# Kernel optimization log

Hardware: AMD Instinct MI355X
Metric: run time of the kernel (lower is better)

Reference implementation:

```python
import jax, jax.numpy as jnp
import numpy as np

EPS = jnp.finfo(jnp.float32).eps


def setup_inputs() -> dict:
    key = jax.random.key(0)
    k0, k1, k2 = jax.random.split(key, 3)
    B, N = 1, 4194304
    cloud_t0 = jax.random.normal(k0, (B, N, 3), dtype=jnp.float32)
    cloud_t1 = jax.random.normal(k1, (B, N, 3), dtype=jnp.float32)
    weights = jax.random.uniform(k2, (B, N), dtype=jnp.float32)
    return {"cloud_t0": cloud_t0, "cloud_t1": cloud_t1, "weights": weights}


def reference(cloud_t0, cloud_t1, weights):
    # use_epsilon_on_weights = False branch
    count_nonzero = jnp.sum(weights > 0.0, axis=-1)
    not_enough_points = count_nonzero < 3
    weights = weights + (not_enough_points.astype(weights.dtype) * EPS)[:, None]

    cum_wts = jnp.sum(weights, axis=-1)                      # (B,)
    w = weights[:, :, None]                                   # (B,N,1)
    mx = jnp.sum(cloud_t0 * w, axis=1) / cum_wts[:, None]     # (B,3) weighted centroid
    my = jnp.sum(cloud_t1 * w, axis=1) / cum_wts[:, None]
    Xc = cloud_t0 - mx[:, None, :]
    Yc = cloud_t1 - my[:, None, :]
    # weighted cross-covariance: (B,3,3)
    Sxy = jnp.einsum('bno,bni->boi', Yc * w, Xc) / cum_wts[:, None, None]

    U, D, Vh = jnp.linalg.svd(Sxy, full_matrices=False)       # torch.svd returns V = Vh^T
    V = jnp.swapaxes(Vh, -1, -2)

    # rank via torch.linalg.matrix_rank default tol: max_sv * max(m,n) * eps
    tol = D.max(axis=-1) * 3 * EPS
    rank = jnp.sum(D > tol[:, None], axis=-1)

    det_S = jnp.linalg.det(Sxy)
    det_mul = jnp.linalg.det(U) * jnp.linalg.det(V)
    sign_full = jnp.where(det_S < 0.0, -1.0, 1.0)             # rank == 3 case
    sign_def = jnp.where(jnp.isclose(det_mul, -1.0), -1.0, 1.0)  # rank == 2 case
    s = jnp.where(rank > 2, sign_full, sign_def)              # (B,)

    # R = U @ diag(1,1,s) @ V^T
    diag = jnp.stack([jnp.ones_like(s), jnp.ones_like(s), s], axis=-1)  # (B,3)
    R = jnp.einsum('boc,bc,bic->boi', U, diag, V)             # (B,3,3)
    t = my - jnp.einsum('boc,bc->bo', R, mx)                  # (B,3)

    B = R.shape[0]
    R4 = jnp.concatenate([R, jnp.zeros((B, 1, 3), R.dtype)], axis=1)    # (B,4,3)
    t4 = jnp.concatenate([t, jnp.ones((B, 1), t.dtype)], axis=-1)       # (B,4)
    T = jnp.concatenate([R4, t4[:, :, None]], axis=-1)        # (B,4,4)
    return T, not_enough_points
```

## Files before the change

### kernel.cpp

```cpp
#include <hip/hip_runtime.h>
#include <math.h>

#define NACC 32
#define NMAIN 17
#define NFALL 15

__device__ __forceinline__ void accum_main(float w, float x0, float x1, float x2,
                                           float y0, float y1, float y2, float* a) {
    a[0] += (w > 0.0f) ? 1.0f : 0.0f;
    a[1] += w;
    a[2] = fmaf(w, x0, a[2]); a[3] = fmaf(w, x1, a[3]); a[4] = fmaf(w, x2, a[4]);
    float wy0 = w * y0, wy1 = w * y1, wy2 = w * y2;
    a[5] += wy0; a[6] += wy1; a[7] += wy2;
    a[8]  = fmaf(wy0, x0, a[8]);  a[9]  = fmaf(wy0, x1, a[9]);  a[10] = fmaf(wy0, x2, a[10]);
    a[11] = fmaf(wy1, x0, a[11]); a[12] = fmaf(wy1, x1, a[12]); a[13] = fmaf(wy1, x2, a[13]);
    a[14] = fmaf(wy2, x0, a[14]); a[15] = fmaf(wy2, x1, a[15]); a[16] = fmaf(wy2, x2, a[16]);
}

__device__ __forceinline__ void accum_fall(float x0, float x1, float x2,
                                           float y0, float y1, float y2, float* f) {
    f[0] += x0; f[1] += x1; f[2] += x2;
    f[3] += y0; f[4] += y1; f[5] += y2;
    f[6]  = fmaf(y0, x0, f[6]);  f[7]  = fmaf(y0, x1, f[7]);  f[8]  = fmaf(y0, x2, f[8]);
    f[9]  = fmaf(y1, x0, f[9]);  f[10] = fmaf(y1, x1, f[10]); f[11] = fmaf(y1, x2, f[11]);
    f[12] = fmaf(y2, x0, f[12]); f[13] = fmaf(y2, x1, f[13]); f[14] = fmaf(y2, x2, f[14]);
}

__device__ __forceinline__ void accum_group_main(float4 wv, float4 x0, float4 x1, float4 x2,
                                                 float4 y0, float4 y1, float4 y2, float* a) {
    accum_main(wv.x, x0.x, x0.y, x0.z, y0.x, y0.y, y0.z, a);
    accum_main(wv.y, x0.w, x1.x, x1.y, y0.w, y1.x, y1.y, a);
    accum_main(wv.z, x1.z, x1.w, x2.x, y1.z, y1.w, y2.x, a);
    accum_main(wv.w, x2.y, x2.z, x2.w, y2.y, y2.z, y2.w, a);
}

__device__ __forceinline__ void accum_group_fall(float4 x0, float4 x1, float4 x2,
                                                 float4 y0, float4 y1, float4 y2, float* f) {
    accum_fall(x0.x, x0.y, x0.z, y0.x, y0.y, y0.z, f);
    accum_fall(x0.w, x1.x, x1.y, y0.w, y1.x, y1.y, f);
    accum_fall(x1.z, x1.w, x2.x, y1.z, y1.w, y2.x, f);
    accum_fall(x2.y, x2.z, x2.w, y2.y, y2.z, y2.w, f);
}

template <int NV>
__device__ __forceinline__ void block_reduce(float* v, float (*sm)[NACC], int t) {
    int wave = t >> 6, lane = t & 63;
    #pragma unroll
    for (int off = 32; off > 0; off >>= 1) {
        #pragma unroll
        for (int i = 0; i < NV; ++i) v[i] += __shfl_down(v[i], off, 64);
    }
    if (lane == 0) {
        #pragma unroll
        for (int i = 0; i < NV; ++i) sm[wave][i] = v[i];
    }
    __syncthreads();
}

__global__ __launch_bounds__(256) void kabsch_reduce(
    const float* __restrict__ c0, const float* __restrict__ c1,
    const float* __restrict__ w, int N, float* __restrict__ partials, int nblocks) {
    __shared__ float sm[4][NACC];

    float a[NMAIN];
    #pragma unroll
    for (int i = 0; i < NMAIN; ++i) a[i] = 0.0f;

    const int t = threadIdx.x;
    const int tid = blockIdx.x * blockDim.x + t;
    const int nthreads = gridDim.x * blockDim.x;
    const int ngroups = N >> 2;
    const float4* A4 = (const float4*)c0;
    const float4* B4 = (const float4*)c1;
    const float4* W4 = (const float4*)w;

    int g = tid;
    bool have = g < ngroups;
    float4 cw, ca0, ca1, ca2, cb0, cb1, cb2;
    if (have) {
        size_t b = (size_t)3 * (size_t)g;
        cw = W4[g];
        ca0 = A4[b]; ca1 = A4[b + 1]; ca2 = A4[b + 2];
        cb0 = B4[b]; cb1 = B4[b + 1]; cb2 = B4[b + 2];
    }
    while (have) {
        int gn = g + nthreads;
        bool haven = gn < ngroups;
        float4 nw, na0, na1, na2, nb0, nb1, nb2;
        if (haven) {
            size_t b = (size_t)3 * (size_t)gn;
            nw = W4[gn];
            na0 = A4[b]; na1 = A4[b + 1]; na2 = A4[b + 2];
            nb0 = B4[b]; nb1 = B4[b + 1]; nb2 = B4[b + 2];
        }
        accum_group_main(cw, ca0, ca1, ca2, cb0, cb1, cb2, a);
        cw = nw; ca0 = na0; ca1 = na1; ca2 = na2; cb0 = nb0; cb1 = nb1; cb2 = nb2;
        g = gn; have = haven;
    }
    if (tid == 0) {
        for (int i = (ngroups << 2); i < N; ++i)
            accum_main(w[i], c0[3*i], c0[3*i+1], c0[3*i+2],
                       c1[3*i], c1[3*i+1], c1[3*i+2], a);
    }

    block_reduce<NMAIN>(a, sm, t);
    float blockCnt = sm[0][0] + sm[1][0] + sm[2][0] + sm[3][0];
    if (t < NMAIN)
        partials[t * nblocks + blockIdx.x] =
            sm[0][t] + sm[1][t] + sm[2][t] + sm[3][t];

    if (blockCnt >= 3.0f) {
        __syncthreads();
        if (t < NFALL) partials[(NMAIN + t) * nblocks + blockIdx.x] = 0.0f;
        return;
    }
    float f[NFALL];
    #pragma unroll
    for (int i = 0; i < NFALL; ++i) f[i] = 0.0f;
    for (int gg = tid; gg < ngroups; gg += nthreads) {
        size_t b = (size_t)3 * (size_t)gg;
        accum_group_fall(A4[b], A4[b + 1], A4[b + 2],
                         B4[b], B4[b + 1], B4[b + 2], f);
    }
    if (tid == 0) {
        for (int i = (ngroups << 2); i < N; ++i)
            accum_fall(c0[3*i], c0[3*i+1], c0[3*i+2],
                       c1[3*i], c1[3*i+1], c1[3*i+2], f);
    }
    __syncthreads();
    block_reduce<NFALL>(f, sm, t);
    if (t < NFALL)
        partials[(NMAIN + t) * nblocks + blockIdx.x] =
            sm[0][t] + sm[1][t] + sm[2][t] + sm[3][t];
}

__device__ __forceinline__ double det3(const double m[3][3]) {
    return m[0][0] * (m[1][1] * m[2][2] - m[1][2] * m[2][1])
         - m[0][1] * (m[1][0] * m[2][2] - m[1][2] * m[2][0])
         + m[0][2] * (m[1][0] * m[2][1] - m[1][1] * m[2][0]);
}

__global__ __launch_bounds__(256) void kabsch_finalize(
    const float* __restrict__ partials, int nblocks, int N, float* __restrict__ out) {
    double d[NACC];
    #pragma unroll
    for (int i = 0; i < NACC; ++i) d[i] = 0.0;
    for (int m = threadIdx.x; m < nblocks; m += 256) {
        #pragma unroll
        for (int i = 0; i < NACC; ++i)
            d[i] += (double)partials[i * nblocks + m];
    }
    #pragma unroll
    for (int off = 32; off > 0; off >>= 1) {
        #pragma unroll
        for (int i = 0; i < NACC; ++i) d[i] += __shfl_down(d[i], off, 64);
    }
    __shared__ double sm[4][NACC];
    int wave = threadIdx.x >> 6, lane = threadIdx.x & 63;
    if (lane == 0) {
        #pragma unroll
        for (int i = 0; i < NACC; ++i) sm[wave][i] = d[i];
    }
    __syncthreads();
    if (threadIdx.x != 0) return;
    #pragma unroll
    for (int i = 0; i < NACC; ++i) d[i] = sm[0][i] + sm[1][i] + sm[2][i] + sm[3][i];

    const double EPSF = (double)1.1920929e-7f;
    double cnt = d[0];
    double W = d[1];
    double swx[3] = { d[2], d[3], d[4] };
    double swy[3] = { d[5], d[6], d[7] };
    double swyx[9];
    for (int i = 0; i < 9; ++i) swyx[i] = d[8 + i];
    bool nep = cnt < 3.0;
    if (nep) {
        W += EPSF * (double)N;
        for (int i = 0; i < 3; ++i) { swx[i] += EPSF * d[17 + i]; swy[i] += EPSF * d[20 + i]; }
        for (int i = 0; i < 9; ++i) swyx[i] += EPSF * d[23 + i];
    }

    double mx[3], my[3];
    for (int i = 0; i < 3; ++i) { mx[i] = swx[i] / W; my[i] = swy[i] / W; }
    double S[3][3];
    for (int o = 0; o < 3; ++o)
        for (int i = 0; i < 3; ++i)
            S[o][i] = swyx[o * 3 + i] / W - my[o] * mx[i];

    double Bm[3][3], V[3][3];
    for (int i = 0; i < 3; ++i)
        for (int j = 0; j < 3; ++j) {
            double acc = 0.0;
            for (int k = 0; k < 3; ++k) acc += S[k][i] * S[k][j];
            Bm[i][j] = acc;
            V[i][j] = (i == j) ? 1.0 : 0.0;
        }
    for (int sweep = 0; sweep < 6; ++sweep) {
        for (int pair = 0; pair < 3; ++pair) {
            int p = (pair == 2) ? 1 : 0;
            int q = (pair == 0) ? 1 : 2;
            double apq = Bm[p][q];
            if (fabs(apq) < 1e-300) continue;
            double theta = (Bm[q][q] - Bm[p][p]) / (2.0 * apq);
            double tt = ((theta >= 0.0) ? 1.0 : -1.0) / (fabs(theta) + sqrt(1.0 + theta * theta));
            double c = 1.0 / sqrt(1.0 + tt * tt);
            double sn = tt * c;
            for (int k = 0; k < 3; ++k) {
                double bkp = Bm[k][p], bkq = Bm[k][q];
                Bm[k][p] = c * bkp - sn * bkq;
                Bm[k][q] = sn * bkp + c * bkq;
            }
            for (int k = 0; k < 3; ++k) {
                double bpk = Bm[p][k], bqk = Bm[q][k];
                Bm[p][k] = c * bpk - sn * bqk;
                Bm[q][k] = sn * bpk + c * bqk;
            }
            for (int k = 0; k < 3; ++k) {
                double vkp = V[k][p], vkq = V[k][q];
                V[k][p] = c * vkp - sn * vkq;
                V[k][q] = sn * vkp + c * vkq;
            }
        }
    }
    double lam[3] = { Bm[0][0], Bm[1][1], Bm[2][2] };
    for (int i = 0; i < 2; ++i)
        for (int j = i + 1; j < 3; ++j)
            if (lam[j] > lam[i]) {
                double tl = lam[i]; lam[i] = lam[j]; lam[j] = tl;
                for (int k = 0; k < 3; ++k) { double tv = V[k][i]; V[k][i] = V[k][j]; V[k][j] = tv; }
            }
    double sig[3];
    for (int i = 0; i < 3; ++i) sig[i] = sqrt(fmax(lam[i], 0.0));

    double U[3][3];
    for (int i = 0; i < 3; ++i) {
        double u0 = S[0][0]*V[0][i] + S[0][1]*V[1][i] + S[0][2]*V[2][i];
        double u1 = S[1][0]*V[0][i] + S[1][1]*V[1][i] + S[1][2]*V[2][i];
        double u2 = S[2][0]*V[0][i] + S[2][1]*V[1][i] + S[2][2]*V[2][i];
        double nrm = sqrt(u0*u0 + u1*u1 + u2*u2);
        if (nrm > 1e-150) {
            U[0][i] = u0 / nrm; U[1][i] = u1 / nrm; U[2][i] = u2 / nrm;
        } else if (i == 0) {
            U[0][0] = 1.0; U[1][0] = 0.0; U[2][0] = 0.0;
        } else if (i == 1) {
            double e0 = (fabs(U[0][0]) < 0.9) ? 1.0 : 0.0;
            double e1 = 1.0 - e0;
            double dp = e0 * U[0][0] + e1 * U[1][0];
            double v0 = e0 - dp * U[0][0], v1 = e1 - dp * U[1][0], v2 = -dp * U[2][0];
            double n2 = sqrt(v0*v0 + v1*v1 + v2*v2);
            U[0][1] = v0 / n2; U[1][1] = v1 / n2; U[2][1] = v2 / n2;
        } else {
            U[0][2] = U[1][0]*U[2][1] - U[2][0]*U[1][1];
            U[1][2] = U[2][0]*U[0][1] - U[0][0]*U[2][1];
            U[2][2] = U[0][0]*U[1][1] - U[1][0]*U[0][1];
        }
    }

    double tol = sig[0] * 3.0 * EPSF;
    int rank = (sig[0] > tol) + (sig[1] > tol) + (sig[2] > tol);
    double detS = det3(S);
    double det_mul = det3(U) * det3(V);
    double sign_full = (detS < 0.0) ? -1.0 : 1.0;
    double sign_def = (fabs(det_mul + 1.0) <= 1.00001e-5) ? -1.0 : 1.0;
    double s = (rank > 2) ? sign_full : sign_def;

    double R[3][3];
    for (int o = 0; o < 3; ++o)
        for (int i = 0; i < 3; ++i)
            R[o][i] = U[o][0]*V[i][0] + U[o][1]*V[i][1] + s * U[o][2]*V[i][2];
    double tv[3];
    for (int o = 0; o < 3; ++o)
        tv[o] = my[o] - (R[o][0]*mx[0] + R[o][1]*mx[1] + R[o][2]*mx[2]);

    for (int o = 0; o < 3; ++o) {
        out[o * 4 + 0] = (float)R[o][0];
        out[o * 4 + 1] = (float)R[o][1];
        out[o * 4 + 2] = (float)R[o][2];
        out[o * 4 + 3] = (float)tv[o];
    }
    out[12] = 0.0f; out[13] = 0.0f; out[14] = 0.0f; out[15] = 1.0f;
    out[16] = nep ? 1.0f : 0.0f;
}

extern "C" void kernel_launch(void* const* d_in, const int* in_sizes, int n_in,
                              void* d_out, int out_size, void* d_ws, size_t ws_size,
                              hipStream_t stream) {
    const float* c0 = (const float*)d_in[0];
    const float* c1 = (const float*)d_in[1];
    const float* w  = (const float*)d_in[2];
    float* out = (float*)d_out;
    int N = in_sizes[2];

    int blocks = 2048;
    size_t need = (size_t)blocks * NACC * sizeof(float);
    if (need > ws_size) {
        blocks = (int)(ws_size / (NACC * sizeof(float)));
        if (blocks < 1) blocks = 1;
    }
    float* partials = (float*)d_ws;

    kabsch_reduce<<<blocks, 256, 0, stream>>>(c0, c1, w, N, partials, blocks);
    kabsch_finalize<<<1, 256, 0, stream>>>(partials, blocks, N, out);
}
```

Measured before the change: 155.9 us.

## Stage point tiles into LDS via async global_load_lds with double buffering

```diff
diff --git a/kernel.cpp b/kernel.cpp
--- a/kernel.cpp
+++ b/kernel.cpp
@@ -2,6 +2,7 @@
 #include <math.h>
 
 #define NACC 32
+#define TILE 1024
 #define NMAIN 17
 #define NFALL 15
 
@@ -42,6 +43,13 @@
     accum_fall(x2.y, x2.z, x2.w, y2.y, y2.z, y2.w, f);
 }
 
+__device__ __forceinline__ void gl2lds16(const float* g_perlane, float* lds_uniform) {
+    __builtin_amdgcn_global_load_lds(
+        (const __attribute__((address_space(1))) void*)g_perlane,
+        (__attribute__((address_space(3))) void*)lds_uniform,
+        16, 0, 0);
+}
+
 template <int NV>
 __device__ __forceinline__ void block_reduce(float* v, float (*sm)[NACC], int t) {
     int wave = t >> 6, lane = t & 63;
@@ -60,6 +68,8 @@
 __global__ __launch_bounds__(256) void kabsch_reduce(
     const float* __restrict__ c0, const float* __restrict__ c1,
     const float* __restrict__ w, int N, float* __restrict__ partials, int nblocks) {
+    __shared__ float sA[2][TILE * 3];
+    __shared__ float sB[2][TILE * 3];
     __shared__ float sm[4][NACC];
 
     float a[NMAIN];
@@ -67,56 +77,76 @@
     for (int i = 0; i < NMAIN; ++i) a[i] = 0.0f;
 
     const int t = threadIdx.x;
+    const int wave = t >> 6, lane = t & 63;
+    const int ntiles = N >> 10;
+    const float4* W4 = (const float4*)w;
+
+    int k = blockIdx.x;
+    bool have = k < ntiles;
+    int buf = 0;
+    float4 wcur;
+    if (have) {
+        const float* ga = c0 + (size_t)k * 3072;
+        const float* gb = c1 + (size_t)k * 3072;
+        #pragma unroll
+        for (int c = 0; c < 3; ++c) {
+            int chunk = wave * 3 + c;
+            gl2lds16(ga + chunk * 256 + lane * 4, &sA[0][chunk * 256]);
+            gl2lds16(gb + chunk * 256 + lane * 4, &sB[0][chunk * 256]);
+        }
+        wcur = W4[(size_t)k * 256 + t];
+    }
+    while (have) {
+        int kn = k + gridDim.x;
+        bool haven = kn < ntiles;
+        __syncthreads();
+        float4 wnext;
+        if (haven) {
+            const float* ga = c0 + (size_t)kn * 3072;
+            const float* gb = c1 + (size_t)kn * 3072;
+            #pragma unroll
+            for (int c = 0; c < 3; ++c) {
+                int chunk = wave * 3 + c;
+                gl2lds16(ga + chunk * 256 + lane * 4, &sA[buf ^ 1][chunk * 256]);
+                gl2lds16(gb + chunk * 256 + lane * 4, &sB[buf ^ 1][chunk * 256]);
+            }
+            wnext = W4[(size_t)kn * 256 + t];
+        }
+        {
+            const float4* pa = (const float4*)(&sA[buf][t * 12]);
+            const float4* pb = (const float4*)(&sB[buf][t * 12]);
+            float4 xa0 = pa[0], xa1 = pa[1], xa2 = pa[2];
+            float4 xb0 = pb[0], xb1 = pb[1], xb2 = pb[2];
+            accum_group_main(wcur, xa0, xa1, xa2, xb0, xb1, xb2, a);
+        }
+        wcur = wnext; k = kn; have = haven; buf ^= 1;
+    }
+    if (blockIdx.x == 0 && t == 0) {
+        for (int i = ntiles << 10; i < N; ++i)
+            accum_main(w[i], c0[3*i], c0[3*i+1], c0[3*i+2],
+                       c1[3*i], c1[3*i+1], c1[3*i+2], a);
+    }
+
+    __syncthreads();
+    block_reduce<NMAIN>(a, sm, t);
+    float blockCnt = sm[0][0] + sm[1][0] + sm[2][0] + sm[3][0];
+    if (t < NMAIN)
+        partials[t * nblocks + blockIdx.x] =
+            sm[0][t] + sm[1][t] + sm[2][t] + sm[3][t];
+
+    if (blockCnt >= 3.0f) {
+        __syncthreads();
+        if (t < NFALL) partials[(NMAIN + t) * nblocks + blockIdx.x] = 0.0f;
+        return;
+    }
+    float f[NFALL];
+    #pragma unroll
+    for (int i = 0; i < NFALL; ++i) f[i] = 0.0f;
     const int tid = blockIdx.x * blockDim.x + t;
     const int nthreads = gridDim.x * blockDim.x;
     const int ngroups = N >> 2;
     const float4* A4 = (const float4*)c0;
     const float4* B4 = (const float4*)c1;
-    const float4* W4 = (const float4*)w;
-
-    int g = tid;
-    bool have = g < ngroups;
-    float4 cw, ca0, ca1, ca2, cb0, cb1, cb2;
-    if (have) {
-        size_t b = (size_t)3 * (size_t)g;
-        cw = W4[g];
-        ca0 = A4[b]; ca1 = A4[b + 1]; ca2 = A4[b + 2];
-        cb0 = B4[b]; cb1 = B4[b + 1]; cb2 = B4[b + 2];
-    }
-    while (have) {
-        int gn = g + nthreads;
-        bool haven = gn < ngroups;
-        float4 nw, na0, na1, na2, nb0, nb1, nb2;
-        if (haven) {
-            size_t b = (size_t)3 * (size_t)gn;
-            nw = W4[gn];
-            na0 = A4[b]; na1 = A4[b + 1]; na2 = A4[b + 2];
-            nb0 = B4[b]; nb1 = B4[b + 1]; nb2 = B4[b + 2];
-        }
-        accum_group_main(cw, ca0, ca1, ca2, cb0, cb1, cb2, a);
-        cw = nw; ca0 = na0; ca1 = na1; ca2 = na2; cb0 = nb0; cb1 = nb1; cb2 = nb2;
-        g = gn; have = haven;
-    }
-    if (tid == 0) {
-        for (int i = (ngroups << 2); i < N; ++i)
-            accum_main(w[i], c0[3*i], c0[3*i+1], c0[3*i+2],
-                       c1[3*i], c1[3*i+1], c1[3*i+2], a);
-    }
-
-    block_reduce<NMAIN>(a, sm, t);
-    float blockCnt = sm[0][0] + sm[1][0] + sm[2][0] + sm[3][0];
-    if (t < NMAIN)
-        partials[t * nblocks + blockIdx.x] =
-            sm[0][t] + sm[1][t] + sm[2][t] + sm[3][t];
-
-    if (blockCnt >= 3.0f) {
-        __syncthreads();
-        if (t < NFALL) partials[(NMAIN + t) * nblocks + blockIdx.x] = 0.0f;
-        return;
-    }
-    float f[NFALL];
-    #pragma unroll
-    for (int i = 0; i < NFALL; ++i) f[i] = 0.0f;
     for (int gg = tid; gg < ngroups; gg += nthreads) {
         size_t b = (size_t)3 * (size_t)gg;
         accum_group_fall(A4[b], A4[b + 1], A4[b + 2],
@@ -291,7 +321,7 @@
     float* out = (float*)d_out;
     int N = in_sizes[2];
 
-    int blocks = 2048;
+    int blocks = 768;
     size_t need = (size_t)blocks * NACC * sizeof(float);
     if (need > ws_size) {
         blocks = (int)(ws_size / (NACC * sizeof(float)));
```

After: 154.5 us. Within noise of the previous version (-0.9%).
